# Optimization experiments

Hardware: AMD Instinct MI355X
Metric: run time of the kernel (lower is better)

Reference implementation:

```python
import jax, jax.numpy as jnp
import numpy as np

B, S, H = 4, 512, 256

def setup_inputs() -> dict:
    key = jax.random.key(0)
    k1, k2, k3, k4 = jax.random.split(key, 4)
    scale = 1.0 / np.sqrt(H)
    return {
        "h": jax.random.normal(k1, (B, S, H), dtype=jnp.float32),
        "W_t": jax.random.normal(k2, (H, H), dtype=jnp.float32) * scale,
        "W_t_prime": jax.random.normal(k3, (H, H), dtype=jnp.float32) * scale,
        "b_h": jnp.zeros((H,), dtype=jnp.float32),
        "W_a": jax.random.normal(k4, (H,), dtype=jnp.float32) * scale,
        "b_a": jnp.zeros((), dtype=jnp.float32),
    }

def reference(h, W_t, W_t_prime, b_h, W_a, b_a):
    # Project once per timestep, then broadcast-add over the (t, t') pair grid.
    ht = jnp.einsum("bsh,hk->bsk", h, W_t)          # W_t applied to h^t
    htp = jnp.einsum("bsh,hk->bsk", h, W_t_prime)   # W_{t'} applied to h^{t'}
    # transformed: (B, S_t, S_t', H)
    transformed = ht[:, :, None, :] + htp[:, None, :, :] + b_h
    tanh_out = jnp.tanh(transformed)
    scores = jnp.einsum("bsth,h->bst", tanh_out, W_a) + b_a  # (B, S, S)
    scores = jax.nn.sigmoid(scores)
    attention_weights = jax.nn.softmax(scores, axis=2)
    output = jnp.einsum("bst,bth->bsh", attention_weights, h)
    return output, attention_weights
```

## Files before the change

### kernel.cpp

```cpp
#include <hip/hip_runtime.h>

#define Bn 4
#define Sn 512
#define Hn 256

#define CC   2.8853900817779268f
#define L2E  1.4426950408889634f

typedef __attribute__((ext_vector_type(4))) float f32x4;
typedef __attribute__((ext_vector_type(8))) short short8;

__device__ __forceinline__ unsigned short bf16rn(float f) {
    unsigned int u = __float_as_uint(f);
    u += 0x7fffu + ((u >> 16) & 1u);
    return (unsigned short)(u >> 16);
}
__device__ __forceinline__ float bf16tof(unsigned short b) {
    return __uint_as_float(((unsigned int)b) << 16);
}

__global__ __launch_bounds__(256) void prep_kernel(
    const float* __restrict__ h,  const float* __restrict__ Wt,
    const float* __restrict__ Wp, const float* __restrict__ Wa,
    const float* __restrict__ ba,
    unsigned short* __restrict__ h1, unsigned short* __restrict__ h2,
    unsigned short* __restrict__ wtp,
    float* __restrict__ wa2, float* __restrict__ cst)
{
    __shared__ float tile[64 * 68];
    __shared__ float red4[4];
    const int tid = threadIdx.x;
    const int bid = blockIdx.x;

    if (bid < 256) {
        const int base = (bid * 256 + tid) * 8;
        float4 v0 = *(const float4*)&h[base];
        float4 v1 = *(const float4*)&h[base + 4];
        float f[8] = {v0.x, v0.y, v0.z, v0.w, v1.x, v1.y, v1.z, v1.w};
        unsigned short b1[8], b2[8];
#pragma unroll
        for (int i = 0; i < 8; i++) {
            b1[i] = bf16rn(f[i]);
            b2[i] = bf16rn(f[i] - bf16tof(b1[i]));
        }
        uint4 u1, u2;
        u1.x = (unsigned)b1[0] | ((unsigned)b1[1] << 16);
        u1.y = (unsigned)b1[2] | ((unsigned)b1[3] << 16);
        u1.z = (unsigned)b1[4] | ((unsigned)b1[5] << 16);
        u1.w = (unsigned)b1[6] | ((unsigned)b1[7] << 16);
        u2.x = (unsigned)b2[0] | ((unsigned)b2[1] << 16);
        u2.y = (unsigned)b2[2] | ((unsigned)b2[3] << 16);
        u2.z = (unsigned)b2[4] | ((unsigned)b2[5] << 16);
        u2.w = (unsigned)b2[6] | ((unsigned)b2[7] << 16);
        *(uint4*)&h1[base] = u1;
        *(uint4*)&h2[base] = u2;

        if (bid == 0) {
            float w = Wa[tid];
#pragma unroll
            for (int off = 32; off >= 1; off >>= 1) w += __shfl_xor(w, off, 64);
            if ((tid & 63) == 0) red4[tid >> 6] = w;
            __syncthreads();
            wa2[tid] = -2.0f * Wa[tid];
            if (tid == 0)
                cst[0] = -L2E * ((red4[0] + red4[1] + red4[2] + red4[3]) + ba[0]);
        }
    } else {
        const int sb  = bid - 256;
        const int mat = sb >> 4;
        const int t4  = sb & 15;
        const int k0  = (t4 >> 2) * 64, n0 = (t4 & 3) * 64;
        const float* __restrict__ W = mat ? Wp : Wt;

#pragma unroll
        for (int i = 0; i < 4; i++) {
            const int idx = tid + 256 * i;
            const int kr = idx >> 4, nq = idx & 15;
            *(float4*)&tile[kr * 68 + nq * 4] =
                *(const float4*)&W[(k0 + kr) * Hn + n0 + nq * 4];
        }
        __syncthreads();

        unsigned short* p1 = wtp + mat * 2 * 65536;
        unsigned short* p2 = p1 + 65536;
#pragma unroll
        for (int i = 0; i < 8; i++) {
            const int idx = tid + 256 * i;
            const int n = idx >> 5, kp = idx & 31;
            const float f0 = tile[(2 * kp) * 68 + n];
            const float f1 = tile[(2 * kp + 1) * 68 + n];
            const unsigned short a0 = bf16rn(f0), a1 = bf16rn(f1);
            const unsigned short c0 = bf16rn(f0 - bf16tof(a0));
            const unsigned short c1 = bf16rn(f1 - bf16tof(a1));
            const int dw = ((n0 + n) * 256 + k0) / 2 + kp;
            ((unsigned int*)p1)[dw] = (unsigned)a0 | ((unsigned)a1 << 16);
            ((unsigned int*)p2)[dw] = (unsigned)c0 | ((unsigned)c1 << 16);
        }
    }
}

__global__ __launch_bounds__(256) void gemm_kernel(
    const unsigned short* __restrict__ h1, const unsigned short* __restrict__ h2,
    const unsigned short* __restrict__ wtp, const float* __restrict__ bh,
    float* __restrict__ Egt, float* __restrict__ Egp4)
{
    __shared__ char lds[20480];

    const int tid = threadIdx.x;
    const int mb = blockIdx.x >> 3;
    const int nb = blockIdx.x & 7;
    const int m0 = mb * 64;
    const bool isT = (nb < 4);
    const int n0l = isT ? nb * 64 : (nb - 4) * 64;
    const unsigned short* pB1 = wtp + (isT ? 0 : 2 * 65536);
    const unsigned short* pB2 = pB1 + 65536;

    const int w    = tid >> 6;
    const int lane = tid & 63;
    const int quad = lane >> 4;
    const int l15  = lane & 15;

    f32x4 acc[4];
#pragma unroll
    for (int i = 0; i < 4; i++) acc[i] = (f32x4){0.f, 0.f, 0.f, 0.f};

    const int ssel = tid >> 7;
    const int spl  = (tid >> 6) & 1;
    const int srow = (tid & 63) >> 2;
    const int sseg = tid & 3;
    const unsigned short* gsrc =
        (ssel == 0) ? (spl ? h2 : h1) : (spl ? pB2 : pB1);
    const int growbase = (ssel == 0) ? m0 : n0l;
    char* ldsdst = lds + (ssel * 2 + spl) * 5120;

    for (int ks = 0; ks < 256; ks += 32) {
        __syncthreads();
#pragma unroll
        for (int i = 0; i < 4; i++) {
            const int row = srow + i * 16;
            uint4 v = *(const uint4*)&gsrc[(growbase + row) * 256 + ks + sseg * 8];
            *(uint4*)(ldsdst + row * 80 + sseg * 16) = v;
        }
        __syncthreads();

        const char* Ab = lds;
        const char* Bb = lds + 10240;
        const short8 b1 = *(const short8*)(Bb + (w * 16 + l15) * 80 + quad * 16);
        const short8 b2 = *(const short8*)(Bb + 5120 + (w * 16 + l15) * 80 + quad * 16);
#pragma unroll
        for (int mt = 0; mt < 4; mt++) {
            const short8 a1 = *(const short8*)(Ab + (mt * 16 + l15) * 80 + quad * 16);
            const short8 a2 = *(const short8*)(Ab + 5120 + (mt * 16 + l15) * 80 + quad * 16);
            acc[mt] = __builtin_amdgcn_mfma_f32_16x16x32_bf16(a1, b1, acc[mt], 0, 0, 0);
            acc[mt] = __builtin_amdgcn_mfma_f32_16x16x32_bf16(a1, b2, acc[mt], 0, 0, 0);
            acc[mt] = __builtin_amdgcn_mfma_f32_16x16x32_bf16(a2, b1, acc[mt], 0, 0, 0);
        }
    }

    __syncthreads();
    float* ct = (float*)lds;
#pragma unroll
    for (int mt = 0; mt < 4; mt++)
#pragma unroll
        for (int r = 0; r < 4; r++)
            ct[(mt * 16 + quad * 4 + r) * 68 + w * 16 + l15] = acc[mt][r];
    __syncthreads();

    const int b  = m0 >> 9;
    const int s0 = m0 & 511;
    if (isT) {
        const int n0g = nb * 64;
#pragma unroll
        for (int i = 0; i < 4; i++) {
            const int item = tid + i * 256;
            const int mr = item >> 4, nq = item & 15;
            const float4 c  = *(const float4*)&ct[mr * 68 + nq * 4];
            const float4 bv = *(const float4*)&bh[n0g + nq * 4];
            float4 o;
            o.x = __builtin_amdgcn_exp2f((c.x + bv.x) * CC);
            o.y = __builtin_amdgcn_exp2f((c.y + bv.y) * CC);
            o.z = __builtin_amdgcn_exp2f((c.z + bv.z) * CC);
            o.w = __builtin_amdgcn_exp2f((c.w + bv.w) * CC);
            *(float4*)&Egt[(m0 + mr) * Hn + n0g + nq * 4] = o;
        }
    } else {
        const int kq0 = (nb - 4) * 16;
#pragma unroll
        for (int i = 0; i < 4; i++) {
            const int item = tid + i * 256;
            const int mr = item & 63, nq = item >> 6;
            const float4 c = *(const float4*)&ct[mr * 68 + nq * 4];
            float4 o;
            o.x = __builtin_amdgcn_exp2f(c.x * CC);
            o.y = __builtin_amdgcn_exp2f(c.y * CC);
            o.z = __builtin_amdgcn_exp2f(c.z * CC);
            o.w = __builtin_amdgcn_exp2f(c.w * CC);
            *(float4*)&Egp4[b * 131072 + (kq0 + nq) * 2048 + (s0 + mr) * 4] = o;
        }
    }
}

__global__ __launch_bounds__(512) void attn_kernel(
    const float* __restrict__ hsrc, const float* __restrict__ Egt,
    const float* __restrict__ Egp4, const float* __restrict__ wa2,
    const float* __restrict__ cst,
    float* __restrict__ out, float* __restrict__ out_attn)
{
    __shared__ char smem[49152];
    float*  egt8   = (float*)smem;
    float*  attn_l = (float*)smem;
    float*  wal    = (float*)(smem + 16384);
    float*  red    = (float*)(smem + 17408);
    float4* part   = (float4*)(smem + 16384);

    const int tid = threadIdx.x;
    const int b   = blockIdx.x & 3;
    const int t0  = (blockIdx.x >> 2) << 3;

    for (int i = tid; i < 8 * Hn; i += 512)
        egt8[i] = Egt[(b * Sn + t0) * Hn + i];
    if (tid < 256) wal[tid] = wa2[tid];
    __syncthreads();

    const float4* __restrict__ ep = (const float4*)(Egp4 + b * (Hn * Sn));

    float acc[8];
#pragma unroll
    for (int r = 0; r < 8; r++) acc[r] = 0.f;

    float4 cur = ep[tid];
    float4 nxt = ep[Sn + tid];
    for (int k4 = 0; k4 < 64; k4++) {
        const float4 nn = ep[((k4 + 2) & 63) * Sn + tid];
        const float4 w4 = *(const float4*)&wal[k4 * 4];
#pragma unroll
        for (int r = 0; r < 8; r++) {
            const float4 eg = *(const float4*)&egt8[r * Hn + k4 * 4];
            const float d1 = fmaf(cur.x, eg.x, 1.0f);
            const float d2 = fmaf(cur.y, eg.y, 1.0f);
            const float d3 = fmaf(cur.z, eg.z, 1.0f);
            const float d4 = fmaf(cur.w, eg.w, 1.0f);
            const float p12 = d1 * d2, p34 = d3 * d4;
            const float n12 = fmaf(w4.x, d2, w4.y * d1);
            const float n34 = fmaf(w4.z, d4, w4.w * d3);
            const float num = fmaf(n12, p34, n34 * p12);
            acc[r] = fmaf(num, __builtin_amdgcn_rcpf(p12 * p34), acc[r]);
        }
        cur = nxt; nxt = nn;
    }

    const float k0 = cst[0];
    float ex[8];
#pragma unroll
    for (int r = 0; r < 8; r++) {
        const float e1  = __builtin_amdgcn_exp2f(fmaf(-L2E, acc[r], k0));
        const float sig = __builtin_amdgcn_rcpf(1.0f + e1);
        ex[r] = __builtin_amdgcn_exp2f(L2E * sig);
    }

    const int lane = tid & 63, wid = tid >> 6;
#pragma unroll
    for (int r = 0; r < 8; r++) {
        float v = ex[r];
#pragma unroll
        for (int off = 32; off >= 1; off >>= 1) v += __shfl_xor(v, off, 64);
        if (lane == 0) red[r * 8 + wid] = v;
    }
    __syncthreads();

#pragma unroll
    for (int r = 0; r < 8; r++) {
        float tot = 0.f;
#pragma unroll
        for (int i = 0; i < 8; i++) tot += red[r * 8 + i];
        const float a = ex[r] * __builtin_amdgcn_rcpf(tot);
        attn_l[r * Sn + tid] = a;
        out_attn[(b * Sn + t0 + r) * Sn + tid] = a;
    }
    __syncthreads();

    const int c4 = tid & 63;
    const int q  = __builtin_amdgcn_readfirstlane(tid >> 6);

    const float* __restrict__ hb = hsrc + (b * Sn + q * 64) * Hn + c4 * 4;

    float4 a[8];
#pragma unroll
    for (int r = 0; r < 8; r++) a[r] = (float4){0.f, 0.f, 0.f, 0.f};

#pragma unroll 2
    for (int j4 = 0; j4 < 16; j4++) {
        float4 wv[8];
#pragma unroll
        for (int r = 0; r < 8; r++)
            wv[r] = *(const float4*)&attn_l[r * Sn + q * 64 + j4 * 4];
#pragma unroll
        for (int i = 0; i < 4; i++) {
            const float4 hv = *(const float4*)&hb[(j4 * 4 + i) * Hn];
#pragma unroll
            for (int r = 0; r < 8; r++) {
                const float wr = ((const float*)&wv[r])[i];
                a[r].x = fmaf(wr, hv.x, a[r].x);
                a[r].y = fmaf(wr, hv.y, a[r].y);
                a[r].z = fmaf(wr, hv.z, a[r].z);
                a[r].w = fmaf(wr, hv.w, a[r].w);
            }
        }
    }
    __syncthreads();

    if (q < 4) {
#pragma unroll
        for (int r = 0; r < 8; r++) part[(q * 8 + r) * 64 + c4] = a[r];
    }
    __syncthreads();
    if (q >= 4) {
#pragma unroll
        for (int r = 0; r < 8; r++) {
            float4 p = part[((q - 4) * 8 + r) * 64 + c4];
            p.x += a[r].x; p.y += a[r].y; p.z += a[r].z; p.w += a[r].w;
            part[((q - 4) * 8 + r) * 64 + c4] = p;
        }
    }
    __syncthreads();

    const int col = tid & 255;
    const int rs  = tid >> 8;
    const float* pf = (const float*)part;
#pragma unroll
    for (int rr = 0; rr < 4; rr++) {
        const int r = rs * 4 + rr;
        float s = 0.f;
#pragma unroll
        for (int qq = 0; qq < 4; qq++)
            s += pf[((qq * 8 + r) * 64 + (col >> 2)) * 4 + (col & 3)];
        out[(b * Sn + t0 + r) * Hn + col] = s;
    }
}

extern "C" void kernel_launch(void* const* d_in, const int* in_sizes, int n_in,
                              void* d_out, int out_size, void* d_ws, size_t ws_size,
                              hipStream_t stream) {
    const float* h   = (const float*)d_in[0];
    const float* Wt  = (const float*)d_in[1];
    const float* Wtp = (const float*)d_in[2];
    const float* bh  = (const float*)d_in[3];
    const float* Wa  = (const float*)d_in[4];
    const float* ba  = (const float*)d_in[5];

    float* out      = (float*)d_out;
    float* out_attn = out + Bn * Sn * Hn;

    float* ws   = (float*)d_ws;
    float* Egt  = ws;
    float* Egp4 = ws + 524288;
    float* wa2  = ws + 1048576;
    float* cst  = ws + 1048832;
    unsigned short* h1  = (unsigned short*)(ws + 1048840);
    unsigned short* h2  = h1 + 2048 * 256;
    unsigned short* wtp = h2 + 2048 * 256;

    prep_kernel<<<dim3(288), dim3(256), 0, stream>>>(
        h, Wt, Wtp, Wa, ba, h1, h2, wtp, wa2, cst);
    gemm_kernel<<<dim3(256), dim3(256), 0, stream>>>(h1, h2, wtp, bh, Egt, Egp4);
    attn_kernel<<<dim3(Bn * (Sn / 8)), dim3(512), 0, stream>>>(
        h, Egt, Egp4, wa2, cst, out, out_attn);
}
```

Before: 125.1 us.

## Halve rows per attention block and use packed float2 math in score loop

```diff
diff --git a/kernel.cpp b/kernel.cpp
--- a/kernel.cpp
+++ b/kernel.cpp
@@ -8,6 +8,7 @@
 #define L2E  1.4426950408889634f
 
 typedef __attribute__((ext_vector_type(4))) float f32x4;
+typedef __attribute__((ext_vector_type(2))) float f32x2;
 typedef __attribute__((ext_vector_type(8))) short short8;
 
 __device__ __forceinline__ unsigned short bf16rn(float f) {
@@ -206,61 +207,68 @@
     const float* __restrict__ cst,
     float* __restrict__ out, float* __restrict__ out_attn)
 {
-    __shared__ char smem[49152];
-    float*  egt8   = (float*)smem;
+    __shared__ char smem[26624];
+    float*  egt4   = (float*)smem;
     float*  attn_l = (float*)smem;
-    float*  wal    = (float*)(smem + 16384);
-    float*  red    = (float*)(smem + 17408);
-    float4* part   = (float4*)(smem + 16384);
+    float*  wal    = (float*)(smem + 8192);
+    float*  red    = (float*)(smem + 9472);
+    float4* part   = (float4*)(smem + 10240);
 
     const int tid = threadIdx.x;
     const int b   = blockIdx.x & 3;
-    const int t0  = (blockIdx.x >> 2) << 3;
-
-    for (int i = tid; i < 8 * Hn; i += 512)
-        egt8[i] = Egt[(b * Sn + t0) * Hn + i];
+    const int t0  = (blockIdx.x >> 2) << 2;
+
+    for (int i = tid; i < 4 * Hn; i += 512)
+        egt4[i] = Egt[(b * Sn + t0) * Hn + i];
     if (tid < 256) wal[tid] = wa2[tid];
     __syncthreads();
 
     const float4* __restrict__ ep = (const float4*)(Egp4 + b * (Hn * Sn));
 
-    float acc[8];
-#pragma unroll
-    for (int r = 0; r < 8; r++) acc[r] = 0.f;
+    f32x2 accA[4], accB[4];
+#pragma unroll
+    for (int r = 0; r < 4; r++) { accA[r] = (f32x2){0.f, 0.f}; accB[r] = (f32x2){0.f, 0.f}; }
 
     float4 cur = ep[tid];
     float4 nxt = ep[Sn + tid];
     for (int k4 = 0; k4 < 64; k4++) {
         const float4 nn = ep[((k4 + 2) & 63) * Sn + tid];
         const float4 w4 = *(const float4*)&wal[k4 * 4];
-#pragma unroll
-        for (int r = 0; r < 8; r++) {
-            const float4 eg = *(const float4*)&egt8[r * Hn + k4 * 4];
-            const float d1 = fmaf(cur.x, eg.x, 1.0f);
-            const float d2 = fmaf(cur.y, eg.y, 1.0f);
-            const float d3 = fmaf(cur.z, eg.z, 1.0f);
-            const float d4 = fmaf(cur.w, eg.w, 1.0f);
-            const float p12 = d1 * d2, p34 = d3 * d4;
-            const float n12 = fmaf(w4.x, d2, w4.y * d1);
-            const float n34 = fmaf(w4.z, d4, w4.w * d3);
-            const float num = fmaf(n12, p34, n34 * p12);
-            acc[r] = fmaf(num, __builtin_amdgcn_rcpf(p12 * p34), acc[r]);
+        const f32x2 wa01 = (f32x2){w4.x, w4.y};
+        const f32x2 wa23 = (f32x2){w4.z, w4.w};
+        const f32x2 ep01 = (f32x2){cur.x, cur.y};
+        const f32x2 ep23 = (f32x2){cur.z, cur.w};
+#pragma unroll
+        for (int r = 0; r < 4; r++) {
+            const float4 eg = *(const float4*)&egt4[r * Hn + k4 * 4];
+            const f32x2 d01 = ep01 * (f32x2){eg.x, eg.y} + (f32x2){1.f, 1.f};
+            const f32x2 d23 = ep23 * (f32x2){eg.z, eg.w} + (f32x2){1.f, 1.f};
+            const float p01 = d01.x * d01.y;
+            const float p23 = d23.x * d23.y;
+            const float rr  = __builtin_amdgcn_rcpf(p01 * p23);
+            const float q23 = p23 * rr;
+            const float q01 = p01 * rr;
+            const f32x2 m01 = wa01 * (f32x2){d01.y, d01.x};
+            const f32x2 m23 = wa23 * (f32x2){d23.y, d23.x};
+            accA[r] = accA[r] + m01 * (f32x2){q23, q23};
+            accB[r] = accB[r] + m23 * (f32x2){q01, q01};
         }
         cur = nxt; nxt = nn;
     }
 
     const float k0 = cst[0];
-    float ex[8];
-#pragma unroll
-    for (int r = 0; r < 8; r++) {
-        const float e1  = __builtin_amdgcn_exp2f(fmaf(-L2E, acc[r], k0));
+    float ex[4];
+#pragma unroll
+    for (int r = 0; r < 4; r++) {
+        const float a = (accA[r].x + accA[r].y) + (accB[r].x + accB[r].y);
+        const float e1  = __builtin_amdgcn_exp2f(fmaf(-L2E, a, k0));
         const float sig = __builtin_amdgcn_rcpf(1.0f + e1);
         ex[r] = __builtin_amdgcn_exp2f(L2E * sig);
     }
 
     const int lane = tid & 63, wid = tid >> 6;
 #pragma unroll
-    for (int r = 0; r < 8; r++) {
+    for (int r = 0; r < 4; r++) {
         float v = ex[r];
 #pragma unroll
         for (int off = 32; off >= 1; off >>= 1) v += __shfl_xor(v, off, 64);
@@ -269,7 +277,7 @@
     __syncthreads();
 
 #pragma unroll
-    for (int r = 0; r < 8; r++) {
+    for (int r = 0; r < 4; r++) {
         float tot = 0.f;
 #pragma unroll
         for (int i = 0; i < 8; i++) tot += red[r * 8 + i];
@@ -284,21 +292,21 @@
 
     const float* __restrict__ hb = hsrc + (b * Sn + q * 64) * Hn + c4 * 4;
 
-    float4 a[8];
-#pragma unroll
-    for (int r = 0; r < 8; r++) a[r] = (float4){0.f, 0.f, 0.f, 0.f};
+    float4 a[4];
+#pragma unroll
+    for (int r = 0; r < 4; r++) a[r] = (float4){0.f, 0.f, 0.f, 0.f};
 
 #pragma unroll 2
     for (int j4 = 0; j4 < 16; j4++) {
-        float4 wv[8];
-#pragma unroll
-        for (int r = 0; r < 8; r++)
+        float4 wv[4];
+#pragma unroll
+        for (int r = 0; r < 4; r++)
             wv[r] = *(const float4*)&attn_l[r * Sn + q * 64 + j4 * 4];
 #pragma unroll
         for (int i = 0; i < 4; i++) {
             const float4 hv = *(const float4*)&hb[(j4 * 4 + i) * Hn];
 #pragma unroll
-            for (int r = 0; r < 8; r++) {
+            for (int r = 0; r < 4; r++) {
                 const float wr = ((const float*)&wv[r])[i];
                 a[r].x = fmaf(wr, hv.x, a[r].x);
                 a[r].y = fmaf(wr, hv.y, a[r].y);
@@ -311,29 +319,29 @@
 
     if (q < 4) {
 #pragma unroll
-        for (int r = 0; r < 8; r++) part[(q * 8 + r) * 64 + c4] = a[r];
+        for (int r = 0; r < 4; r++) part[(q * 4 + r) * 64 + c4] = a[r];
     }
     __syncthreads();
     if (q >= 4) {
 #pragma unroll
-        for (int r = 0; r < 8; r++) {
-            float4 p = part[((q - 4) * 8 + r) * 64 + c4];
+        for (int r = 0; r < 4; r++) {
+            float4 p = part[((q - 4) * 4 + r) * 64 + c4];
             p.x += a[r].x; p.y += a[r].y; p.z += a[r].z; p.w += a[r].w;
-            part[((q - 4) * 8 + r) * 64 + c4] = p;
+            part[((q - 4) * 4 + r) * 64 + c4] = p;
         }
     }
     __syncthreads();
 
     const int col = tid & 255;
-    const int rs  = tid >> 8;
+    const int rh  = tid >> 8;
     const float* pf = (const float*)part;
 #pragma unroll
-    for (int rr = 0; rr < 4; rr++) {
-        const int r = rs * 4 + rr;
+    for (int rr = 0; rr < 2; rr++) {
+        const int r = rh * 2 + rr;
         float s = 0.f;
 #pragma unroll
         for (int qq = 0; qq < 4; qq++)
-            s += pf[((qq * 8 + r) * 64 + (col >> 2)) * 4 + (col & 3)];
+            s += pf[((qq * 4 + r) * 64 + (col >> 2)) * 4 + (col & 3)];
         out[(b * Sn + t0 + r) * Hn + col] = s;
     }
 }
@@ -363,6 +371,6 @@
     prep_kernel<<<dim3(288), dim3(256), 0, stream>>>(
         h, Wt, Wtp, Wa, ba, h1, h2, wtp, wa2, cst);
     gemm_kernel<<<dim3(256), dim3(256), 0, stream>>>(h1, h2, wtp, bh, Egt, Egp4);
-    attn_kernel<<<dim3(Bn * (Sn / 8)), dim3(512), 0, stream>>>(
+    attn_kernel<<<dim3(Bn * (Sn / 4)), dim3(512), 0, stream>>>(
         h, Egt, Egp4, wa2, cst, out, out_attn);
 }
```

Measured after the change: 124.2 us. About the same (-0.8%).
